# Kernel tuning notes

Hardware: AMD Instinct MI355X
Metric: run time of the kernel (lower is better)

The kernel has to match this reference:

```python
import jax, jax.numpy as jnp
import numpy as np

R = 32
BN_EPS = 1e-5

def _bn(x, g, b, m, v, axis=1):
    shp = [1] * x.ndim
    shp[axis] = -1
    return (x - m.reshape(shp)) * (g.reshape(shp) / jnp.sqrt(v.reshape(shp) + BN_EPS)) + b.reshape(shp)

def _voxelize(features, coords, r):
    # features [B,C,N], coords [B,3,N] -> vox [B,C,r,r,r], norm_coords [B,3,N] in [0,r-1]
    B, C, N = features.shape
    c = coords - coords.mean(axis=2, keepdims=True)
    scale = jnp.linalg.norm(c, axis=1).max(axis=1)  # [B] max point radius
    c = c / (scale[:, None, None] * 2.0) + 0.5      # normalize=True, eps=0
    norm_coords = jnp.clip(c * r, 0.0, r - 1)
    idx = jnp.round(norm_coords).astype(jnp.int32)  # [B,3,N]
    flat = (jnp.arange(B, dtype=jnp.int32)[:, None] * (r ** 3)
            + idx[:, 0] * r * r + idx[:, 1] * r + idx[:, 2]).reshape(-1)  # [B*N]
    feats = features.transpose(0, 2, 1).reshape(B * N, C)
    sums = jax.ops.segment_sum(feats, flat, num_segments=B * r ** 3)
    cnts = jax.ops.segment_sum(jnp.ones((B * N,), features.dtype), flat, num_segments=B * r ** 3)
    avg = sums / jnp.maximum(cnts, 1.0)[:, None]
    vox = avg.reshape(B, r, r, r, C).transpose(0, 4, 1, 2, 3)
    return vox, norm_coords

def _devoxelize(vox, coords, r):
    # vox [B,C,r,r,r], coords [B,3,N] float in [0,r-1] -> [B,C,N]
    B = vox.shape[0]
    lo = jnp.floor(coords)
    frac = coords - lo
    lo = lo.astype(jnp.int32)
    hi = jnp.minimum(lo + 1, r - 1)
    bidx = jnp.arange(B)[:, None]
    def g(ix, iy, iz):
        return vox[bidx, :, ix, iy, iz]  # [B,N,C]
    x0, y0, z0 = lo[:, 0], lo[:, 1], lo[:, 2]
    x1, y1, z1 = hi[:, 0], hi[:, 1], hi[:, 2]
    fx, fy, fz = frac[:, 0], frac[:, 1], frac[:, 2]
    out = (g(x0, y0, z0) * ((1 - fx) * (1 - fy) * (1 - fz))[..., None]
         + g(x0, y0, z1) * ((1 - fx) * (1 - fy) * fz)[..., None]
         + g(x0, y1, z0) * ((1 - fx) * fy * (1 - fz))[..., None]
         + g(x0, y1, z1) * ((1 - fx) * fy * fz)[..., None]
         + g(x1, y0, z0) * (fx * (1 - fy) * (1 - fz))[..., None]
         + g(x1, y0, z1) * (fx * (1 - fy) * fz)[..., None]
         + g(x1, y1, z0) * (fx * fy * (1 - fz))[..., None]
         + g(x1, y1, z1) * (fx * fy * fz)[..., None])
    return out.transpose(0, 2, 1)

def _conv3d(x, w, b):
    y = jax.lax.conv_general_dilated(x, w, (1, 1, 1), 'SAME',
                                     dimension_numbers=('NCDHW', 'OIDHW', 'NCDHW'))
    return y + b[None, :, None, None, None]

def setup_inputs() -> dict:
    key = jax.random.key(0)
    ks = jax.random.split(key, 24)
    B, Cin, Cout, N = 8, 64, 64, 65536
    d = {
        'features': jax.random.normal(ks[0], (B, Cin, N), jnp.float32),
        'coords': jax.random.normal(ks[1], (B, 3, N), jnp.float32),
        'time_emb': jax.random.normal(ks[2], (B, 64), jnp.float32),
        'conv1_w': jax.random.normal(ks[3], (Cout, Cin, 3, 3, 3), jnp.float32) * 0.05,
        'conv1_b': jax.random.normal(ks[4], (Cout,), jnp.float32) * 0.05,
        'bn1_g': jax.random.uniform(ks[5], (Cout,), jnp.float32, 0.5, 1.5),
        'bn1_b': jax.random.normal(ks[6], (Cout,), jnp.float32) * 0.05,
        'bn1_m': jax.random.normal(ks[7], (Cout,), jnp.float32) * 0.05,
        'bn1_v': jax.random.uniform(ks[8], (Cout,), jnp.float32, 0.5, 1.5),
        'conv2_w': jax.random.normal(ks[9], (Cout, Cout, 3, 3, 3), jnp.float32) * 0.05,
        'conv2_b': jax.random.normal(ks[10], (Cout,), jnp.float32) * 0.05,
        'bn2_g': jax.random.uniform(ks[11], (Cout,), jnp.float32, 0.5, 1.5),
        'bn2_b': jax.random.normal(ks[12], (Cout,), jnp.float32) * 0.05,
        'bn2_m': jax.random.normal(ks[13], (Cout,), jnp.float32) * 0.05,
        'bn2_v': jax.random.uniform(ks[14], (Cout,), jnp.float32, 0.5, 1.5),
        'mlp_w': jax.random.normal(ks[15], (Cout, Cin), jnp.float32) * 0.1,
        'mlp_b': jax.random.normal(ks[16], (Cout,), jnp.float32) * 0.05,
        'bn3_g': jax.random.uniform(ks[17], (Cout,), jnp.float32, 0.5, 1.5),
        'bn3_b': jax.random.normal(ks[18], (Cout,), jnp.float32) * 0.05,
        'bn3_m': jax.random.normal(ks[19], (Cout,), jnp.float32) * 0.05,
        'bn3_v': jax.random.uniform(ks[20], (Cout,), jnp.float32, 0.5, 1.5),
    }
    return d

def reference(features, coords, time_emb,
              conv1_w, conv1_b, bn1_g, bn1_b, bn1_m, bn1_v,
              conv2_w, conv2_b, bn2_g, bn2_b, bn2_m, bn2_v,
              mlp_w, mlp_b, bn3_g, bn3_b, bn3_m, bn3_v):
    vox, vcoords = _voxelize(features, coords, R)
    x = jax.nn.silu(_bn(_conv3d(vox, conv1_w, conv1_b), bn1_g, bn1_b, bn1_m, bn1_v))
    x = jax.nn.silu(_bn(_conv3d(x, conv2_w, conv2_b), bn2_g, bn2_b, bn2_m, bn2_v))  # use_attention=False -> SiLU
    devox = _devoxelize(x, vcoords, R)  # [B,Cout,N]
    pt = jnp.einsum('oi,bin->bon', mlp_w, features) + mlp_b[None, :, None]
    pt = jax.nn.relu(_bn(pt, bn3_g, bn3_b, bn3_m, bn3_v))  # SharedMLP: Conv1d+BN1d+ReLU
    fused = devox + pt
    return (fused, coords, time_emb)
```

## Files before the change

kernel.cpp:

```cpp
#include <hip/hip_runtime.h>
#include <hip/hip_bf16.h>
#include <math.h>

#define B_   8
#define C_   64
#define N_   65536
#define R_   32
#define R3_  32768
#define RP_  34
#define RP2_ 1156
#define RP3_ 39304

typedef short short8v __attribute__((ext_vector_type(8)));
typedef float floatx4 __attribute__((ext_vector_type(4)));

__device__ inline float bf2f(short u) {
    return __uint_as_float(((unsigned)(unsigned short)u) << 16);
}
__device__ inline unsigned short f2bf(float f) {
    __hip_bfloat16 h = __float2bfloat16(f);
    return *reinterpret_cast<unsigned short*>(&h);
}
__device__ inline void atomicMaxF(float* addr, float v) {
    atomicMax((unsigned int*)addr, __float_as_uint(v));
}

__global__ __launch_bounds__(256) void k_stats_sum(const float* __restrict__ coords,
                                                   float* __restrict__ stats) {
    int b = blockIdx.y;
    int tid = threadIdx.x;
    const float* cb = coords + (size_t)b * 3 * N_;
    float sx = 0.f, sy = 0.f, sz = 0.f;
    int base = blockIdx.x * 2048;
    for (int k = 0; k < 8; ++k) {
        int n = base + k * 256 + tid;
        sx += cb[n];
        sy += cb[N_ + n];
        sz += cb[2 * N_ + n];
    }
    for (int o = 32; o > 0; o >>= 1) {
        sx += __shfl_down(sx, o);
        sy += __shfl_down(sy, o);
        sz += __shfl_down(sz, o);
    }
    if ((tid & 63) == 0) {
        atomicAdd(&stats[b * 8 + 0], sx);
        atomicAdd(&stats[b * 8 + 1], sy);
        atomicAdd(&stats[b * 8 + 2], sz);
    }
}

__global__ __launch_bounds__(256) void k_stats_max(const float* __restrict__ coords,
                                                   float* __restrict__ stats) {
    int b = blockIdx.y;
    int tid = threadIdx.x;
    const float* cb = coords + (size_t)b * 3 * N_;
    float mx = stats[b * 8 + 0] * (1.f / N_);
    float my = stats[b * 8 + 1] * (1.f / N_);
    float mz = stats[b * 8 + 2] * (1.f / N_);
    float vm = 0.f;
    int base = blockIdx.x * 2048;
    for (int k = 0; k < 8; ++k) {
        int n = base + k * 256 + tid;
        float dx = cb[n] - mx, dy = cb[N_ + n] - my, dz = cb[2 * N_ + n] - mz;
        vm = fmaxf(vm, sqrtf(dx * dx + dy * dy + dz * dz));
    }
    for (int o = 32; o > 0; o >>= 1) vm = fmaxf(vm, __shfl_down(vm, o));
    if ((tid & 63) == 0) atomicMaxF(&stats[b * 8 + 3], vm);
}

__global__ __launch_bounds__(256) void k_transpose(const float* __restrict__ feats,
                                                   unsigned short* __restrict__ featsT) {
    __shared__ float tile[64][65];
    int b = blockIdx.x >> 10;
    int n0 = (blockIdx.x & 1023) * 64;
    int t = threadIdx.x;
    {
        int c = t >> 2, x0 = (t & 3) * 16;
        const float* src = feats + ((size_t)b * 64 + c) * N_ + n0 + x0;
#pragma unroll
        for (int j = 0; j < 4; ++j) {
            float4 v = *(const float4*)(src + j * 4);
            tile[c][x0 + j * 4 + 0] = v.x;
            tile[c][x0 + j * 4 + 1] = v.y;
            tile[c][x0 + j * 4 + 2] = v.z;
            tile[c][x0 + j * 4 + 3] = v.w;
        }
    }
    __syncthreads();
    {
        int n = t >> 2, c0 = (t & 3) * 16;
        short8v s0, s1;
#pragma unroll
        for (int j = 0; j < 8; ++j) s0[j] = (short)f2bf(tile[c0 + j][n]);
#pragma unroll
        for (int j = 0; j < 8; ++j) s1[j] = (short)f2bf(tile[c0 + 8 + j][n]);
        unsigned short* dst = featsT + ((size_t)b * N_ + n0 + n) * 64 + c0;
        *(short8v*)(dst) = s0;
        *(short8v*)(dst + 8) = s1;
    }
}

__global__ __launch_bounds__(256) void k_hist(const float* __restrict__ coords,
                                              const float* __restrict__ stats,
                                              float* __restrict__ ncoords,
                                              unsigned* __restrict__ pvidx,
                                              unsigned* __restrict__ cnt) {
    int p = blockIdx.x * 256 + threadIdx.x;
    int b = p >> 16, n = p & (N_ - 1);
    const float* cb = coords + (size_t)b * 3 * N_;
    float mx = stats[b * 8 + 0] * (1.f / N_);
    float my = stats[b * 8 + 1] * (1.f / N_);
    float mz = stats[b * 8 + 2] * (1.f / N_);
    float s2 = stats[b * 8 + 3] * 2.0f;
    float cv[3] = {cb[n] - mx, cb[N_ + n] - my, cb[2 * N_ + n] - mz};
    int id[3];
#pragma unroll
    for (int d = 0; d < 3; ++d) {
        float t = cv[d] / s2 + 0.5f;
        float nc = fminf(fmaxf(t * (float)R_, 0.f), (float)(R_ - 1));
        ncoords[((size_t)b * 3 + d) * N_ + n] = nc;
        id[d] = (int)rintf(nc);
    }
    unsigned v = (unsigned)(b * R3_ + id[0] * 1024 + id[1] * 32 + id[2]);
    pvidx[p] = v;
    atomicAdd(&cnt[v], 1u);
}

__global__ __launch_bounds__(256) void k_scan1(const unsigned* __restrict__ cnt,
                                               unsigned* __restrict__ lp,
                                               unsigned* __restrict__ btot) {
    __shared__ unsigned sh[256];
    int t = threadIdx.x;
    int i0 = blockIdx.x * 1024 + t * 4;
    uint4 v = *(const uint4*)(cnt + i0);
    unsigned ts = v.x + v.y + v.z + v.w;
    sh[t] = ts;
    __syncthreads();
    for (int off = 1; off < 256; off <<= 1) {
        unsigned u = (t >= off) ? sh[t - off] : 0u;
        __syncthreads();
        sh[t] += u;
        __syncthreads();
    }
    unsigned ex = sh[t] - ts;
    uint4 o;
    o.x = ex;
    o.y = ex + v.x;
    o.z = ex + v.x + v.y;
    o.w = ex + v.x + v.y + v.z;
    *(uint4*)(lp + i0) = o;
    if (t == 255) btot[blockIdx.x] = sh[255];
}

__global__ __launch_bounds__(256) void k_scan2(unsigned* __restrict__ btot,
                                               unsigned* __restrict__ boff) {
    __shared__ unsigned sh[256];
    int t = threadIdx.x;
    unsigned ts = btot[t];
    sh[t] = ts;
    __syncthreads();
    for (int off = 1; off < 256; off <<= 1) {
        unsigned u = (t >= off) ? sh[t - off] : 0u;
        __syncthreads();
        sh[t] += u;
        __syncthreads();
    }
    boff[t] = sh[t] - ts;
}

__global__ __launch_bounds__(256) void k_rank(const unsigned* __restrict__ pvidx,
                                              const unsigned* __restrict__ lp,
                                              const unsigned* __restrict__ boff,
                                              unsigned* __restrict__ cnt,
                                              unsigned* __restrict__ order) {
    int p = blockIdx.x * 256 + threadIdx.x;
    unsigned v = pvidx[p];
    unsigned pos = atomicAdd(&cnt[v], 1u);
    order[lp[v] + boff[v >> 10] + pos] = (unsigned)p;
}

__global__ __launch_bounds__(256) void k_gather(const unsigned* __restrict__ order,
                                                const unsigned short* __restrict__ featsT,
                                                const unsigned* __restrict__ cnt,
                                                const unsigned* __restrict__ lp,
                                                const unsigned* __restrict__ boff,
                                                __hip_bfloat16* __restrict__ P0) {
    int gid = blockIdx.x * 256 + threadIdx.x;
    int v = gid >> 6;
    int lane = threadIdx.x & 63;
    unsigned base = lp[v] + boff[v >> 10];
    unsigned cv = cnt[v];
    float acc = 0.f;
    for (unsigned i = 0; i < cv; ++i) {
        unsigned p = order[base + i];
        acc += bf2f((short)featsT[(size_t)p * 64 + lane]);
    }
    float avg = (cv > 0) ? acc / (float)cv : 0.f;
    int b = v >> 15, loc = v & (R3_ - 1);
    int d0 = loc >> 10, d1 = (loc >> 5) & 31, d2 = loc & 31;
    P0[((size_t)b * RP3_ + (size_t)(d0 + 1) * RP2_ + (d1 + 1) * RP_ + (d2 + 1)) * 64 + lane] =
        __float2bfloat16(avg);
}

__global__ __launch_bounds__(256) void k_wprep(const float* __restrict__ w1,
                                               const float* __restrict__ w2,
                                               __hip_bfloat16* __restrict__ wb,
                                               const float* __restrict__ mw,
                                               float* __restrict__ mwT) {
    int i = blockIdx.x * 256 + threadIdx.x;
    if (i < 2 * 27 * 64 * 64) {
        int conv = i / 110592;
        int r = i % 110592;
        int tap = r >> 12;
        int rr = r & 4095;
        int co = rr >> 6, ci = rr & 63;
        const float* src = conv ? w2 : w1;
        wb[i] = __float2bfloat16(src[(size_t)(co * 64 + ci) * 27 + tap]);
    }
    if (i < 4096) mwT[(i & 63) * 64 + (i >> 6)] = mw[i];
}

__global__ __launch_bounds__(256) void k_conv_mfma(const __hip_bfloat16* __restrict__ pin,
                                                   const __hip_bfloat16* __restrict__ wt,
                                                   const float* __restrict__ cbias,
                                                   const float* __restrict__ g,
                                                   const float* __restrict__ bb,
                                                   const float* __restrict__ bm,
                                                   const float* __restrict__ bv,
                                                   __hip_bfloat16* __restrict__ pout) {
    int wg = blockIdx.x;
    int q = wg & 3, z = (wg >> 2) & 31, b = wg >> 7;
    int tid = threadIdx.x;
    int wave = tid >> 6, lane = tid & 63;
    int l15 = lane & 15, lk = lane >> 4;

    int yv[4], xv[4], Pb[4];
#pragma unroll
    for (int t = 0; t < 4; ++t) {
        yv[t] = q * 8 + wave * 2 + (t >> 1);
        xv[t] = (t & 1) * 16 + l15;
        Pb[t] = (yv[t] * RP_ + xv[t]) * 64 + lk * 8;
    }
    int Pa[4];
#pragma unroll
    for (int m = 0; m < 4; ++m) Pa[m] = (m * 16 + l15) * 64 + lk * 8;

    const __hip_bfloat16* pb = pin + (size_t)b * RP3_ * 64;
    floatx4 acc[4][4];
#pragma unroll
    for (int m = 0; m < 4; ++m)
#pragma unroll
        for (int t = 0; t < 4; ++t) acc[m][t] = (floatx4){0.f, 0.f, 0.f, 0.f};

    for (int tap = 0; tap < 27; ++tap) {
        int dz = tap / 9, dyx = tap % 9, dy = dyx / 3, dx = dyx % 3;
        const __hip_bfloat16* ptap = pb + (size_t)(((z + dz) * RP_ + dy) * RP_ + dx) * 64;
        const __hip_bfloat16* wtap = wt + tap * 4096;
#pragma unroll
        for (int ks = 0; ks < 2; ++ks) {
            short8v a[4], bfr[4];
#pragma unroll
            for (int m = 0; m < 4; ++m)
                a[m] = *(const short8v*)(wtap + Pa[m] + ks * 32);
#pragma unroll
            for (int t = 0; t < 4; ++t)
                bfr[t] = *(const short8v*)(ptap + Pb[t] + ks * 32);
#pragma unroll
            for (int m = 0; m < 4; ++m)
#pragma unroll
                for (int t = 0; t < 4; ++t)
                    acc[m][t] = __builtin_amdgcn_mfma_f32_16x16x32_bf16(a[m], bfr[t], acc[m][t],
                                                                        0, 0, 0);
        }
    }

    __hip_bfloat16* ob = pout + (size_t)b * RP3_ * 64;
#pragma unroll
    for (int m = 0; m < 4; ++m) {
        int cb = m * 16 + lk * 4;
        float4 g4 = *(const float4*)(g + cb);
        float4 b4 = *(const float4*)(bb + cb);
        float4 m4 = *(const float4*)(bm + cb);
        float4 v4 = *(const float4*)(bv + cb);
        float4 bi = *(const float4*)(cbias + cb);
        float s0 = g4.x * rsqrtf(v4.x + 1e-5f), s1 = g4.y * rsqrtf(v4.y + 1e-5f);
        float s2 = g4.z * rsqrtf(v4.z + 1e-5f), s3 = g4.w * rsqrtf(v4.w + 1e-5f);
        float t0 = b4.x - m4.x * s0, t1 = b4.y - m4.y * s1;
        float t2 = b4.z - m4.z * s2, t3 = b4.w - m4.w * s3;
#pragma unroll
        for (int t = 0; t < 4; ++t) {
            float r0 = (acc[m][t][0] + bi.x) * s0 + t0;
            float r1 = (acc[m][t][1] + bi.y) * s1 + t1;
            float r2 = (acc[m][t][2] + bi.z) * s2 + t2;
            float r3 = (acc[m][t][3] + bi.w) * s3 + t3;
            r0 = r0 / (1.0f + expf(-r0));
            r1 = r1 / (1.0f + expf(-r1));
            r2 = r2 / (1.0f + expf(-r2));
            r3 = r3 / (1.0f + expf(-r3));
            unsigned lo = (unsigned)f2bf(r0) | ((unsigned)f2bf(r1) << 16);
            unsigned hi = (unsigned)f2bf(r2) | ((unsigned)f2bf(r3) << 16);
            uint2 pk = {lo, hi};
            *(uint2*)(ob + (size_t)(((z + 1) * RP_ + yv[t] + 1) * RP_ + xv[t] + 1) * 64 + cb) = pk;
        }
    }
}

__global__ __launch_bounds__(256) void k_fuse(const __hip_bfloat16* __restrict__ P2,
                                              const float* __restrict__ ncoords,
                                              const float* __restrict__ feats,
                                              const float* __restrict__ mwT,
                                              const float* __restrict__ mb,
                                              const float* __restrict__ g,
                                              const float* __restrict__ bb,
                                              const float* __restrict__ bm,
                                              const float* __restrict__ bv,
                                              float* __restrict__ out) {
    int p = blockIdx.x * 256 + threadIdx.x;
    int b = p >> 16, n = p & (N_ - 1);

    float c0 = ncoords[((size_t)b * 3 + 0) * N_ + n];
    float c1 = ncoords[((size_t)b * 3 + 1) * N_ + n];
    float c2 = ncoords[((size_t)b * 3 + 2) * N_ + n];
    float fl0 = floorf(c0), fl1 = floorf(c1), fl2 = floorf(c2);
    float f0 = c0 - fl0, f1 = c1 - fl1, f2 = c2 - fl2;
    int a0 = (int)fl0, a1 = (int)fl1, a2 = (int)fl2;
    int h0 = min(a0 + 1, R_ - 1), h1 = min(a1 + 1, R_ - 1), h2 = min(a2 + 1, R_ - 1);

    int pvo[8];
    float wct[8];
    {
        int x0 = a0 + 1, x1 = h0 + 1, y0 = a1 + 1, y1 = h1 + 1, z0 = a2 + 1, z1 = h2 + 1;
        pvo[0] = (x0 * RP_ + y0) * RP_ + z0;  wct[0] = (1 - f0) * (1 - f1) * (1 - f2);
        pvo[1] = (x0 * RP_ + y0) * RP_ + z1;  wct[1] = (1 - f0) * (1 - f1) * f2;
        pvo[2] = (x0 * RP_ + y1) * RP_ + z0;  wct[2] = (1 - f0) * f1 * (1 - f2);
        pvo[3] = (x0 * RP_ + y1) * RP_ + z1;  wct[3] = (1 - f0) * f1 * f2;
        pvo[4] = (x1 * RP_ + y0) * RP_ + z0;  wct[4] = f0 * (1 - f1) * (1 - f2);
        pvo[5] = (x1 * RP_ + y0) * RP_ + z1;  wct[5] = f0 * (1 - f1) * f2;
        pvo[6] = (x1 * RP_ + y1) * RP_ + z0;  wct[6] = f0 * f1 * (1 - f2);
        pvo[7] = (x1 * RP_ + y1) * RP_ + z1;  wct[7] = f0 * f1 * f2;
    }

    float acc[64];
#pragma unroll
    for (int co = 0; co < 64; ++co) acc[co] = 0.f;

    const float* fb = feats + (size_t)b * C_ * N_ + n;
#pragma unroll 4
    for (int ci = 0; ci < 64; ++ci) {
        float f = fb[(size_t)ci * N_];
        const float* wr = mwT + ci * 64;
#pragma unroll
        for (int co = 0; co < 64; ++co) acc[co] += f * wr[co];
    }
#pragma unroll
    for (int co = 0; co < 64; ++co) {
        float s = g[co] * rsqrtf(bv[co] + 1e-5f);
        float tt = bb[co] - bm[co] * s;
        float ptv = (acc[co] + mb[co]) * s + tt;
        acc[co] = fmaxf(ptv, 0.f);
    }

    const __hip_bfloat16* vb = P2 + (size_t)b * RP3_ * 64;
#pragma unroll
    for (int k = 0; k < 8; ++k) {
        const short8v* vp = (const short8v*)(vb + (size_t)pvo[k] * 64);
        float wk = wct[k];
#pragma unroll
        for (int cj = 0; cj < 8; ++cj) {
            short8v v8 = vp[cj];
#pragma unroll
            for (int j = 0; j < 8; ++j) acc[cj * 8 + j] += wk * bf2f(v8[j]);
        }
    }
#pragma unroll
    for (int co = 0; co < 64; ++co)
        out[((size_t)b * C_ + co) * N_ + n] = acc[co];
}

extern "C" void kernel_launch(void* const* d_in, const int* in_sizes, int n_in,
                              void* d_out, int out_size, void* d_ws, size_t ws_size,
                              hipStream_t stream) {
    const float* features = (const float*)d_in[0];
    const float* coords   = (const float*)d_in[1];
    const float* time_emb = (const float*)d_in[2];
    const float* conv1_w  = (const float*)d_in[3];
    const float* conv1_b  = (const float*)d_in[4];
    const float* bn1_g = (const float*)d_in[5];
    const float* bn1_b = (const float*)d_in[6];
    const float* bn1_m = (const float*)d_in[7];
    const float* bn1_v = (const float*)d_in[8];
    const float* conv2_w  = (const float*)d_in[9];
    const float* conv2_b  = (const float*)d_in[10];
    const float* bn2_g = (const float*)d_in[11];
    const float* bn2_b = (const float*)d_in[12];
    const float* bn2_m = (const float*)d_in[13];
    const float* bn2_v = (const float*)d_in[14];
    const float* mlp_w = (const float*)d_in[15];
    const float* mlp_b = (const float*)d_in[16];
    const float* bn3_g = (const float*)d_in[17];
    const float* bn3_b = (const float*)d_in[18];
    const float* bn3_m = (const float*)d_in[19];
    const float* bn3_v = (const float*)d_in[20];
    float* out = (float*)d_out;
    float* ws = (float*)d_ws;

    const size_t OFF_A     = 0;
    const size_t OFF_P0    = 16777216;
    const size_t OFF_NC    = 26839040;
    const size_t OFF_PV    = 28411904;
    const size_t OFF_ORD   = 28936192;
    const size_t OFF_CNT   = 29460480;
    const size_t OFF_LP    = 29722624;
    const size_t OFF_BT    = 29984768;
    const size_t OFF_BOFF  = 29985024;
    const size_t OFF_STATS = 29985280;
    const size_t OFF_WB    = 29985344;
    const size_t OFF_MWT   = 30095936;

    unsigned short* featsT = (unsigned short*)(ws + OFF_A);
    __hip_bfloat16* P1 = (__hip_bfloat16*)(ws + OFF_A);
    __hip_bfloat16* P0 = (__hip_bfloat16*)(ws + OFF_P0);
    __hip_bfloat16* P2 = (__hip_bfloat16*)(ws + OFF_P0);
    float* ncrd  = ws + OFF_NC;
    unsigned* pvidx = (unsigned*)(ws + OFF_PV);
    unsigned* order = (unsigned*)(ws + OFF_ORD);
    unsigned* cnt   = (unsigned*)(ws + OFF_CNT);
    unsigned* lp    = (unsigned*)(ws + OFF_LP);
    unsigned* btot  = (unsigned*)(ws + OFF_BT);
    unsigned* boff  = (unsigned*)(ws + OFF_BOFF);
    float* stats = ws + OFF_STATS;
    __hip_bfloat16* wb = (__hip_bfloat16*)(ws + OFF_WB);
    float* mwT = ws + OFF_MWT;

    hipMemsetAsync(cnt, 0, 262144 * sizeof(unsigned), stream);
    hipMemsetAsync(stats, 0, 64 * sizeof(float), stream);
    hipMemsetAsync(P0, 0, (size_t)B_ * RP3_ * 64 * sizeof(__hip_bfloat16), stream);

    k_wprep<<<dim3(864), 256, 0, stream>>>(conv1_w, conv2_w, wb, mlp_w, mwT);
    k_stats_sum<<<dim3(32, B_), 256, 0, stream>>>(coords, stats);
    k_stats_max<<<dim3(32, B_), 256, 0, stream>>>(coords, stats);
    k_transpose<<<dim3(B_ * 1024), 256, 0, stream>>>(features, featsT);
    k_hist<<<dim3(B_ * N_ / 256), 256, 0, stream>>>(coords, stats, ncrd, pvidx, cnt);
    k_scan1<<<dim3(256), 256, 0, stream>>>(cnt, lp, btot);
    hipMemsetAsync(cnt, 0, 262144 * sizeof(unsigned), stream);
    k_scan2<<<dim3(1), 256, 0, stream>>>(btot, boff);
    k_rank<<<dim3(B_ * N_ / 256), 256, 0, stream>>>(pvidx, lp, boff, cnt, order);
    k_gather<<<dim3(B_ * R3_ / 4), 256, 0, stream>>>(order, featsT, cnt, lp, boff, P0);

    hipMemsetAsync(P1, 0, (size_t)B_ * RP3_ * 64 * sizeof(__hip_bfloat16), stream);
    k_conv_mfma<<<dim3(B_ * 32 * 4), 256, 0, stream>>>(P0, wb, conv1_b, bn1_g, bn1_b, bn1_m,
                                                       bn1_v, P1);
    k_conv_mfma<<<dim3(B_ * 32 * 4), 256, 0, stream>>>(P1, wb + 110592, conv2_b, bn2_g, bn2_b,
                                                       bn2_m, bn2_v, P2);
    k_fuse<<<dim3(B_ * N_ / 256), 256, 0, stream>>>(P2, ncrd, features, mwT, mlp_b, bn3_g, bn3_b,
                                                    bn3_m, bn3_v, out);

    hipMemcpyAsync(out + 33554432, coords, (size_t)(B_ * 3 * N_) * sizeof(float),
                   hipMemcpyDeviceToDevice, stream);
    hipMemcpyAsync(out + 35127296, time_emb, (size_t)(B_ * 64) * sizeof(float),
                   hipMemcpyDeviceToDevice, stream);
}
```

Before: 1.219 ms.

## Split conv and fuse kernels across output-channel halves; unroll gather accumulation

```diff
diff --git a/kernel.cpp b/kernel.cpp
--- a/kernel.cpp
+++ b/kernel.cpp
@@ -191,11 +191,23 @@
     int lane = threadIdx.x & 63;
     unsigned base = lp[v] + boff[v >> 10];
     unsigned cv = cnt[v];
-    float acc = 0.f;
-    for (unsigned i = 0; i < cv; ++i) {
-        unsigned p = order[base + i];
-        acc += bf2f((short)featsT[(size_t)p * 64 + lane]);
-    }
+    float a0 = 0.f, a1 = 0.f, a2 = 0.f, a3 = 0.f;
+    unsigned i = 0;
+    for (; i + 4 <= cv; i += 4) {
+        unsigned p0 = order[base + i];
+        unsigned p1 = order[base + i + 1];
+        unsigned p2 = order[base + i + 2];
+        unsigned p3 = order[base + i + 3];
+        a0 += bf2f((short)featsT[(size_t)p0 * 64 + lane]);
+        a1 += bf2f((short)featsT[(size_t)p1 * 64 + lane]);
+        a2 += bf2f((short)featsT[(size_t)p2 * 64 + lane]);
+        a3 += bf2f((short)featsT[(size_t)p3 * 64 + lane]);
+    }
+    for (; i < cv; ++i) {
+        unsigned p0 = order[base + i];
+        a0 += bf2f((short)featsT[(size_t)p0 * 64 + lane]);
+    }
+    float acc = (a0 + a1) + (a2 + a3);
     float avg = (cv > 0) ? acc / (float)cv : 0.f;
     int b = v >> 15, loc = v & (R3_ - 1);
     int d0 = loc >> 10, d1 = (loc >> 5) & 31, d2 = loc & 31;
@@ -221,15 +233,16 @@
     if (i < 4096) mwT[(i & 63) * 64 + (i >> 6)] = mw[i];
 }
 
-__global__ __launch_bounds__(256) void k_conv_mfma(const __hip_bfloat16* __restrict__ pin,
-                                                   const __hip_bfloat16* __restrict__ wt,
-                                                   const float* __restrict__ cbias,
-                                                   const float* __restrict__ g,
-                                                   const float* __restrict__ bb,
-                                                   const float* __restrict__ bm,
-                                                   const float* __restrict__ bv,
-                                                   __hip_bfloat16* __restrict__ pout) {
+__global__ __launch_bounds__(256, 2) void k_conv_mfma(const __hip_bfloat16* __restrict__ pin,
+                                                      const __hip_bfloat16* __restrict__ wt,
+                                                      const float* __restrict__ cbias,
+                                                      const float* __restrict__ g,
+                                                      const float* __restrict__ bb,
+                                                      const float* __restrict__ bm,
+                                                      const float* __restrict__ bv,
+                                                      __hip_bfloat16* __restrict__ pout) {
     int wg = blockIdx.x;
+    int ch = blockIdx.y;
     int q = wg & 3, z = (wg >> 2) & 31, b = wg >> 7;
     int tid = threadIdx.x;
     int wave = tid >> 6, lane = tid & 63;
@@ -242,43 +255,50 @@
         xv[t] = (t & 1) * 16 + l15;
         Pb[t] = (yv[t] * RP_ + xv[t]) * 64 + lk * 8;
     }
-    int Pa[4];
-#pragma unroll
-    for (int m = 0; m < 4; ++m) Pa[m] = (m * 16 + l15) * 64 + lk * 8;
-
-    const __hip_bfloat16* pb = pin + (size_t)b * RP3_ * 64;
-    floatx4 acc[4][4];
-#pragma unroll
-    for (int m = 0; m < 4; ++m)
+    int Pa[2];
+#pragma unroll
+    for (int m = 0; m < 2; ++m) Pa[m] = (ch * 32 + m * 16 + l15) * 64 + lk * 8;
+
+    const __hip_bfloat16* pb = pin + (size_t)b * RP3_ * 64 + (size_t)z * RP2_ * 64;
+    floatx4 acc[2][4];
+#pragma unroll
+    for (int m = 0; m < 2; ++m)
 #pragma unroll
         for (int t = 0; t < 4; ++t) acc[m][t] = (floatx4){0.f, 0.f, 0.f, 0.f};
 
-    for (int tap = 0; tap < 27; ++tap) {
-        int dz = tap / 9, dyx = tap % 9, dy = dyx / 3, dx = dyx % 3;
-        const __hip_bfloat16* ptap = pb + (size_t)(((z + dz) * RP_ + dy) * RP_ + dx) * 64;
-        const __hip_bfloat16* wtap = wt + tap * 4096;
-#pragma unroll
-        for (int ks = 0; ks < 2; ++ks) {
-            short8v a[4], bfr[4];
-#pragma unroll
-            for (int m = 0; m < 4; ++m)
-                a[m] = *(const short8v*)(wtap + Pa[m] + ks * 32);
-#pragma unroll
-            for (int t = 0; t < 4; ++t)
-                bfr[t] = *(const short8v*)(ptap + Pb[t] + ks * 32);
-#pragma unroll
-            for (int m = 0; m < 4; ++m)
-#pragma unroll
-                for (int t = 0; t < 4; ++t)
-                    acc[m][t] = __builtin_amdgcn_mfma_f32_16x16x32_bf16(a[m], bfr[t], acc[m][t],
-                                                                        0, 0, 0);
+#pragma unroll
+    for (int dz = 0; dz < 3; ++dz) {
+#pragma unroll
+        for (int dy = 0; dy < 3; ++dy) {
+#pragma unroll
+            for (int dx = 0; dx < 3; ++dx) {
+                const __hip_bfloat16* ptap = pb + (size_t)((dz * RP_ + dy) * RP_ + dx) * 64;
+                const __hip_bfloat16* wtap = wt + ((dz * 3 + dy) * 3 + dx) * 4096;
+#pragma unroll
+                for (int ks = 0; ks < 2; ++ks) {
+                    short8v a0 = *(const short8v*)(wtap + Pa[0] + ks * 32);
+                    short8v a1 = *(const short8v*)(wtap + Pa[1] + ks * 32);
+                    short8v b0 = *(const short8v*)(ptap + Pb[0] + ks * 32);
+                    short8v b1 = *(const short8v*)(ptap + Pb[1] + ks * 32);
+                    short8v b2 = *(const short8v*)(ptap + Pb[2] + ks * 32);
+                    short8v b3 = *(const short8v*)(ptap + Pb[3] + ks * 32);
+                    acc[0][0] = __builtin_amdgcn_mfma_f32_16x16x32_bf16(a0, b0, acc[0][0], 0, 0, 0);
+                    acc[0][1] = __builtin_amdgcn_mfma_f32_16x16x32_bf16(a0, b1, acc[0][1], 0, 0, 0);
+                    acc[0][2] = __builtin_amdgcn_mfma_f32_16x16x32_bf16(a0, b2, acc[0][2], 0, 0, 0);
+                    acc[0][3] = __builtin_amdgcn_mfma_f32_16x16x32_bf16(a0, b3, acc[0][3], 0, 0, 0);
+                    acc[1][0] = __builtin_amdgcn_mfma_f32_16x16x32_bf16(a1, b0, acc[1][0], 0, 0, 0);
+                    acc[1][1] = __builtin_amdgcn_mfma_f32_16x16x32_bf16(a1, b1, acc[1][1], 0, 0, 0);
+                    acc[1][2] = __builtin_amdgcn_mfma_f32_16x16x32_bf16(a1, b2, acc[1][2], 0, 0, 0);
+                    acc[1][3] = __builtin_amdgcn_mfma_f32_16x16x32_bf16(a1, b3, acc[1][3], 0, 0, 0);
+                }
+            }
         }
     }
 
     __hip_bfloat16* ob = pout + (size_t)b * RP3_ * 64;
 #pragma unroll
-    for (int m = 0; m < 4; ++m) {
-        int cb = m * 16 + lk * 4;
+    for (int m = 0; m < 2; ++m) {
+        int cb = ch * 32 + m * 16 + lk * 4;
         float4 g4 = *(const float4*)(g + cb);
         float4 b4 = *(const float4*)(bb + cb);
         float4 m4 = *(const float4*)(bm + cb);
@@ -318,6 +338,7 @@
                                               float* __restrict__ out) {
     int p = blockIdx.x * 256 + threadIdx.x;
     int b = p >> 16, n = p & (N_ - 1);
+    int cbase = blockIdx.y * 32;
 
     float c0 = ncoords[((size_t)b * 3 + 0) * N_ + n];
     float c1 = ncoords[((size_t)b * 3 + 1) * N_ + n];
@@ -341,41 +362,42 @@
         pvo[7] = (x1 * RP_ + y1) * RP_ + z1;  wct[7] = f0 * f1 * f2;
     }
 
-    float acc[64];
-#pragma unroll
-    for (int co = 0; co < 64; ++co) acc[co] = 0.f;
+    float acc[32];
+#pragma unroll
+    for (int co = 0; co < 32; ++co) acc[co] = 0.f;
 
     const float* fb = feats + (size_t)b * C_ * N_ + n;
 #pragma unroll 4
     for (int ci = 0; ci < 64; ++ci) {
         float f = fb[(size_t)ci * N_];
-        const float* wr = mwT + ci * 64;
-#pragma unroll
-        for (int co = 0; co < 64; ++co) acc[co] += f * wr[co];
-    }
-#pragma unroll
-    for (int co = 0; co < 64; ++co) {
-        float s = g[co] * rsqrtf(bv[co] + 1e-5f);
-        float tt = bb[co] - bm[co] * s;
-        float ptv = (acc[co] + mb[co]) * s + tt;
+        const float* wr = mwT + ci * 64 + cbase;
+#pragma unroll
+        for (int co = 0; co < 32; ++co) acc[co] += f * wr[co];
+    }
+#pragma unroll
+    for (int co = 0; co < 32; ++co) {
+        int cg = cbase + co;
+        float s = g[cg] * rsqrtf(bv[cg] + 1e-5f);
+        float tt = bb[cg] - bm[cg] * s;
+        float ptv = (acc[co] + mb[cg]) * s + tt;
         acc[co] = fmaxf(ptv, 0.f);
     }
 
-    const __hip_bfloat16* vb = P2 + (size_t)b * RP3_ * 64;
+    const __hip_bfloat16* vb = P2 + (size_t)b * RP3_ * 64 + cbase;
 #pragma unroll
     for (int k = 0; k < 8; ++k) {
         const short8v* vp = (const short8v*)(vb + (size_t)pvo[k] * 64);
         float wk = wct[k];
 #pragma unroll
-        for (int cj = 0; cj < 8; ++cj) {
+        for (int cj = 0; cj < 4; ++cj) {
             short8v v8 = vp[cj];
 #pragma unroll
             for (int j = 0; j < 8; ++j) acc[cj * 8 + j] += wk * bf2f(v8[j]);
         }
     }
 #pragma unroll
-    for (int co = 0; co < 64; ++co)
-        out[((size_t)b * C_ + co) * N_ + n] = acc[co];
+    for (int co = 0; co < 32; ++co)
+        out[((size_t)b * C_ + cbase + co) * N_ + n] = acc[co];
 }
 
 extern "C" void kernel_launch(void* const* d_in, const int* in_sizes, int n_in,
@@ -449,12 +471,12 @@
     k_gather<<<dim3(B_ * R3_ / 4), 256, 0, stream>>>(order, featsT, cnt, lp, boff, P0);
 
     hipMemsetAsync(P1, 0, (size_t)B_ * RP3_ * 64 * sizeof(__hip_bfloat16), stream);
-    k_conv_mfma<<<dim3(B_ * 32 * 4), 256, 0, stream>>>(P0, wb, conv1_b, bn1_g, bn1_b, bn1_m,
-                                                       bn1_v, P1);
-    k_conv_mfma<<<dim3(B_ * 32 * 4), 256, 0, stream>>>(P1, wb + 110592, conv2_b, bn2_g, bn2_b,
-                                                       bn2_m, bn2_v, P2);
-    k_fuse<<<dim3(B_ * N_ / 256), 256, 0, stream>>>(P2, ncrd, features, mwT, mlp_b, bn3_g, bn3_b,
-                                                    bn3_m, bn3_v, out);
+    k_conv_mfma<<<dim3(B_ * 32 * 4, 2), 256, 0, stream>>>(P0, wb, conv1_b, bn1_g, bn1_b, bn1_m,
+                                                          bn1_v, P1);
+    k_conv_mfma<<<dim3(B_ * 32 * 4, 2), 256, 0, stream>>>(P1, wb + 110592, conv2_b, bn2_g, bn2_b,
+                                                          bn2_m, bn2_v, P2);
+    k_fuse<<<dim3(B_ * N_ / 256, 2), 256, 0, stream>>>(P2, ncrd, features, mwT, mlp_b, bn3_g,
+                                                       bn3_b, bn3_m, bn3_v, out);
 
     hipMemcpyAsync(out + 33554432, coords, (size_t)(B_ * 3 * N_) * sizeof(float),
                    hipMemcpyDeviceToDevice, stream);
```

Measured after the change: 1.239 ms. About the same (+1.7%).
